# Performance work log

Measured on AMD Instinct MI355X. Metric: run time of the kernel, lower is better.

The kernel has to match this reference:

```python
import jax, jax.numpy as jnp
import numpy as np

N_HEADS = 8
N_LEVELS = 1
N_POINTS = 4
D_MODEL = 256
BATCH = 2
H0, W0 = 100, 150
LS = H0 * W0
LQ = 15000


def layer_norm(x, g, b, eps=1e-5):
    m = jnp.mean(x, -1, keepdims=True)
    v = jnp.var(x, -1, keepdims=True)
    return (x - m) * jax.lax.rsqrt(v + eps) * g + b


def bilinear_sample(v, Hl, Wl, loc):
    # v: [N, Hl*Wl, Hh, D] level features; loc in [0,1]: [N, Lq, Hh, P, 2] (x, y)
    Nb, _, Hh, D = v.shape
    Lq, P = loc.shape[1], loc.shape[3]
    x = loc[..., 0] * Wl - 0.5           # align_corners=False grid_sample convention
    y = loc[..., 1] * Hl - 0.5
    x0 = jnp.floor(x); y0 = jnp.floor(y)
    lx = (x - x0).transpose(0, 2, 1, 3)[..., None]   # [N,Hh,Lq,P,1]
    ly = (y - y0).transpose(0, 2, 1, 3)[..., None]
    x0i = x0.astype(jnp.int32); y0i = y0.astype(jnp.int32)
    vh = v.transpose(0, 2, 1, 3)                      # [N,Hh,Hl*Wl,D]

    def gather(xi, yi):
        valid = (xi >= 0) & (xi < Wl) & (yi >= 0) & (yi < Hl)   # zero padding
        idx = jnp.clip(yi, 0, Hl - 1) * Wl + jnp.clip(xi, 0, Wl - 1)
        idxf = idx.transpose(0, 2, 1, 3).reshape(Nb, Hh, Lq * P)
        g = jnp.take_along_axis(vh, idxf[..., None], axis=2).reshape(Nb, Hh, Lq, P, D)
        return g * valid.transpose(0, 2, 1, 3)[..., None]

    g00 = gather(x0i, y0i)
    g10 = gather(x0i + 1, y0i)
    g01 = gather(x0i, y0i + 1)
    g11 = gather(x0i + 1, y0i + 1)
    return (g00 * (1 - lx) * (1 - ly) + g10 * lx * (1 - ly)
            + g01 * (1 - lx) * ly + g11 * lx * ly)   # [N,Hh,Lq,P,D]


def ms_deform_attn(q, reference_points, src, shapes_np, starts_np, padding_mask,
                   W_val, b_val, W_off, b_off, W_attn, b_attn, W_out, b_out):
    Nb, Lq, C = q.shape
    Hh, D, L, P = N_HEADS, C // N_HEADS, N_LEVELS, N_POINTS
    value = src @ W_val + b_val
    value = jnp.where(padding_mask[..., None], 0.0, value).reshape(Nb, -1, Hh, D)
    offsets = (q @ W_off + b_off).reshape(Nb, Lq, Hh, L, P, 2)
    aw = jax.nn.softmax((q @ W_attn + b_attn).reshape(Nb, Lq, Hh, L * P), -1)
    aw = aw.reshape(Nb, Lq, Hh, L, P)
    # offset normalizer is (W, H) per level
    norm = jnp.asarray(shapes_np[:, ::-1].copy(), dtype=q.dtype)   # [L,2]
    loc = reference_points[:, :, None, :, None, :] + offsets / norm[None, None, None, :, None, :]
    out = 0.0
    for l in range(L):
        Hl, Wl = int(shapes_np[l, 0]), int(shapes_np[l, 1])
        s = int(starts_np[l])
        sampled = bilinear_sample(value[:, s:s + Hl * Wl], Hl, Wl, loc[:, :, :, l])
        out = out + jnp.sum(sampled * aw[:, :, :, l].transpose(0, 2, 1, 3)[..., None], axis=3)
    out = out.transpose(0, 2, 1, 3).reshape(Nb, Lq, C)
    return out @ W_out + b_out


def reference(tgt, query_pos, src_pos, tgt_spatial_shapes, reference_points,
              depth_reference_points, src, src_spatial_shapes, frame_start_index,
              src_padding_mask,
              W_dsa, b_dsa, g_nds, b_nds, W_off, b_off, W_attn, b_attn,
              W_val, b_val, W_out, b_out, W_csa, b_csa, g_n1, b_n1,
              W_ff, b_ff, g_n3, b_n3):
    ss = np.asarray(src_spatial_shapes)      # static level shapes
    starts = np.asarray(frame_start_index)
    # depth scale adaptation
    src_a = layer_norm(src @ W_dsa + b_dsa, g_nds, b_nds)
    q = tgt + query_pos
    tgt2 = ms_deform_attn(q, reference_points, src_a, ss, starts, src_padding_mask,
                          W_val, b_val, W_off, b_off, W_attn, b_attn, W_out, b_out)
    tgt2 = tgt2 @ W_csa + b_csa
    t = layer_norm(tgt + tgt2, g_n1, b_n1)
    # FFN: single linear d_model->d_model with exact GELU (per source code)
    ff = jax.nn.gelu(t @ W_ff + b_ff, approximate=False)
    return layer_norm(t + ff, g_n3, b_n3)


def setup_inputs() -> dict:
    key = jax.random.key(0)
    ks = jax.random.split(key, 24)
    C = D_MODEL
    Hh, L, P = N_HEADS, N_LEVELS, N_POINTS

    def lin(k, fin, fout, scale=None):
        s = (1.0 / np.sqrt(fin)) if scale is None else scale
        return (jax.random.normal(k, (fin, fout), jnp.float32) * s).astype(jnp.float32)

    inp = {}
    inp['tgt'] = jax.random.normal(ks[0], (BATCH, LQ, C), jnp.float32)
    inp['query_pos'] = 0.1 * jax.random.normal(ks[1], (BATCH, LQ, C), jnp.float32)
    inp['src_pos'] = 0.1 * jax.random.normal(ks[2], (BATCH, LS, C), jnp.float32)
    inp['tgt_spatial_shapes'] = jnp.array([[H0, W0]], jnp.int32)
    inp['reference_points'] = jax.random.uniform(ks[3], (BATCH, LQ, L, 2), jnp.float32)
    inp['depth_reference_points'] = jax.random.uniform(ks[4], (BATCH, LQ, 1, 2), jnp.float32)
    inp['src'] = jax.random.normal(ks[5], (BATCH, LS, C), jnp.float32)
    inp['src_spatial_shapes'] = jnp.array([[H0, W0]], jnp.int32)
    inp['frame_start_index'] = jnp.array([0], jnp.int32)
    inp['src_padding_mask'] = jnp.zeros((BATCH, LS), jnp.bool_)
    # parameters
    inp['W_dsa'] = lin(ks[6], C, C); inp['b_dsa'] = jnp.zeros((C,), jnp.float32)
    inp['g_nds'] = jnp.ones((C,), jnp.float32); inp['b_nds'] = jnp.zeros((C,), jnp.float32)
    inp['W_off'] = lin(ks[7], C, Hh * L * P * 2, scale=0.01)
    inp['b_off'] = 0.5 * jax.random.normal(ks[8], (Hh * L * P * 2,), jnp.float32)
    inp['W_attn'] = lin(ks[9], C, Hh * L * P)
    inp['b_attn'] = jnp.zeros((Hh * L * P,), jnp.float32)
    inp['W_val'] = lin(ks[10], C, C); inp['b_val'] = jnp.zeros((C,), jnp.float32)
    inp['W_out'] = lin(ks[11], C, C); inp['b_out'] = jnp.zeros((C,), jnp.float32)
    inp['W_csa'] = lin(ks[12], C, C); inp['b_csa'] = jnp.zeros((C,), jnp.float32)
    inp['g_n1'] = jnp.ones((C,), jnp.float32); inp['b_n1'] = jnp.zeros((C,), jnp.float32)
    inp['W_ff'] = lin(ks[13], C, C); inp['b_ff'] = jnp.zeros((C,), jnp.float32)
    inp['g_n3'] = jnp.ones((C,), jnp.float32); inp['b_n3'] = jnp.zeros((C,), jnp.float32)
    return inp
```

## Files before the change

kernel.cpp:

```cpp
#include <hip/hip_runtime.h>
#include <hip/hip_bf16.h>
#include <math.h>

#define LQ   15000
#define LS_  15000
#define NB   2
#define ROWS (NB*LQ)
#define HGT  100
#define WID  150
#define KDIM 256

typedef __attribute__((ext_vector_type(8))) short bf16x8;
typedef __attribute__((ext_vector_type(4))) float f32x4;

enum { EP_BIAS_F32 = 0, EP_LN_BF = 1, EP_MASK_HM = 2, EP_RES_LN_BF = 3, EP_GELU_RES_LN_F32 = 4 };
enum { AM_BF16 = 0, AM_F32 = 1, AM_F32SUM = 2 };

__device__ inline short f2bf(float x) {
    __hip_bfloat16 h = __float2bfloat16(x);
    return *reinterpret_cast<short*>(&h);
}
__device__ inline unsigned pack2bf(float a, float b) {
    return ((unsigned)(unsigned short)f2bf(a)) | (((unsigned)(unsigned short)f2bf(b)) << 16);
}
__device__ inline float bf2f(short s) {
    return __uint_as_float(((unsigned)(unsigned short)s) << 16);
}
__device__ inline float gelu_exact(float x) {
    return 0.5f * x * (1.f + erff(x * 0.70710678118654752440f));
}

template<int NT, int EPI, int AMODE>
__global__ __launch_bounds__(256) void mfma_gemm(
    const void* __restrict__ Ap, const void* __restrict__ Ap2,
    const short* __restrict__ WT,
    const float* __restrict__ bias, void* __restrict__ Out,
    const void* __restrict__ Res, const unsigned char* __restrict__ mask,
    const float* __restrict__ lng, const float* __restrict__ lnb, int M)
{
    constexpr int BN = NT * 16;
    __shared__ short As[64][40];
    __shared__ short Bs[BN][40];
    __shared__ float sbias[BN], sg[BN], sb2[BN];

    const int tid  = threadIdx.x;
    const int bm0  = blockIdx.x * 64;
    const int wave = tid >> 6, lane = tid & 63;
    const int quad = lane >> 4, c = lane & 15;

    if (tid < BN) {
        sbias[tid] = bias ? bias[tid] : 0.f;
        if (EPI == EP_LN_BF || EPI == EP_RES_LN_BF || EPI == EP_GELU_RES_LN_F32) {
            sg[tid] = lng[tid]; sb2[tid] = lnb[tid];
        }
    }

    f32x4 acc[NT];
    #pragma unroll
    for (int t = 0; t < NT; ++t) acc[t] = (f32x4){0.f, 0.f, 0.f, 0.f};

    for (int k0 = 0; k0 < KDIM; k0 += 32) {
        if (AMODE != AM_BF16) {
            const float* A  = (const float*)Ap;
            const float* A2 = (const float*)Ap2;
            #pragma unroll
            for (int it = 0; it < 2; ++it) {
                int f = it * 256 + tid; int m = f >> 3; int ko = (f & 7) * 4;
                int r = bm0 + m; if (r > M - 1) r = M - 1;
                float4 v = *(const float4*)&A[(size_t)r * KDIM + k0 + ko];
                if (AMODE == AM_F32SUM) {
                    float4 w = *(const float4*)&A2[(size_t)r * KDIM + k0 + ko];
                    v.x += w.x; v.y += w.y; v.z += w.z; v.w += w.w;
                }
                int2 p; p.x = pack2bf(v.x, v.y); p.y = pack2bf(v.z, v.w);
                *(int2*)&As[m][ko] = p;
            }
        } else {
            const short* A = (const short*)Ap;
            int m = tid >> 2; int ko = (tid & 3) * 8;
            int r = bm0 + m; if (r > M - 1) r = M - 1;
            *(int4*)&As[m][ko] = *(const int4*)&A[(size_t)r * KDIM + k0 + ko];
        }
        #pragma unroll
        for (int it = 0; it < (BN * 4 + 255) / 256; ++it) {
            int f = it * 256 + tid;
            if (f < BN * 4) {
                int n = f >> 2; int ko = (f & 3) * 8;
                *(int4*)&Bs[n][ko] = *(const int4*)&WT[(size_t)n * KDIM + k0 + ko];
            }
        }
        __syncthreads();
        bf16x8 a = *(const bf16x8*)&As[wave * 16 + c][quad * 8];
        #pragma unroll
        for (int t = 0; t < NT; ++t) {
            bf16x8 b = *(const bf16x8*)&Bs[t * 16 + c][quad * 8];
            acc[t] = __builtin_amdgcn_mfma_f32_16x16x32_bf16(a, b, acc[t], 0, 0, 0);
        }
        __syncthreads();
    }

    const int r0 = bm0 + wave * 16 + quad * 4;
    if constexpr (EPI == EP_BIAS_F32) {
        float* O = (float*)Out;
        #pragma unroll
        for (int reg = 0; reg < 4; ++reg) {
            int r = r0 + reg;
            if (r < M) {
                #pragma unroll
                for (int t = 0; t < NT; ++t)
                    O[(size_t)r * BN + t * 16 + c] = acc[t][reg] + sbias[t * 16 + c];
            }
        }
    } else if constexpr (EPI == EP_MASK_HM) {
        short* O = (short*)Out;
        #pragma unroll
        for (int reg = 0; reg < 4; ++reg) {
            int r = r0 + reg;
            if (r < M) {
                float mz = mask[r] ? 0.f : 1.f;
                int n = (r >= LS_) ? 1 : 0;
                int s = r - n * LS_;
                #pragma unroll
                for (int t = 0; t < NT; ++t) {
                    int col = t * 16 + c;
                    int h = col >> 5, d = col & 31;
                    O[(((size_t)n * 8 + h) * LS_ + s) * 32 + d] =
                        f2bf((acc[t][reg] + sbias[col]) * mz);
                }
            }
        }
    } else {
        #pragma unroll
        for (int reg = 0; reg < 4; ++reg) {
            int r = r0 + reg;
            int rl = (r < M) ? r : (M - 1);
            float s = 0.f, sq = 0.f;
            #pragma unroll
            for (int t = 0; t < NT; ++t) {
                float v = acc[t][reg] + sbias[t * 16 + c];
                if constexpr (EPI == EP_GELU_RES_LN_F32) {
                    v = gelu_exact(v);
                    v += bf2f(((const short*)Res)[(size_t)rl * 256 + t * 16 + c]);
                } else if constexpr (EPI == EP_RES_LN_BF) {
                    v += ((const float*)Res)[(size_t)rl * 256 + t * 16 + c];
                }
                acc[t][reg] = v;
                s += v; sq += v * v;
            }
            #pragma unroll
            for (int o = 1; o < 16; o <<= 1) {
                s  += __shfl_xor(s,  o, 64);
                sq += __shfl_xor(sq, o, 64);
            }
            float mean = s * (1.f / 256.f);
            float var  = sq * (1.f / 256.f) - mean * mean;
            float rs   = rsqrtf(var + 1e-5f);
            if (r < M) {
                #pragma unroll
                for (int t = 0; t < NT; ++t) {
                    float o = (acc[t][reg] - mean) * rs * sg[t * 16 + c] + sb2[t * 16 + c];
                    if constexpr (EPI == EP_GELU_RES_LN_F32)
                        ((float*)Out)[(size_t)r * 256 + t * 16 + c] = o;
                    else
                        ((short*)Out)[(size_t)r * 256 + t * 16 + c] = f2bf(o);
                }
            }
        }
    }
}

__global__ __launch_bounds__(256) void transp_cvt(const float* __restrict__ W, short* __restrict__ WT)
{
    __shared__ float tile[64][65];
    int bx = blockIdx.x * 64, by = blockIdx.y * 64;
    int tid = threadIdx.x;
    #pragma unroll
    for (int it = 0; it < 4; ++it) {
        int f = it * 256 + tid; int i = f >> 4; int j = (f & 15) * 4;
        float4 v = *(const float4*)&W[(size_t)(by + i) * 256 + bx + j];
        tile[i][j] = v.x; tile[i][j + 1] = v.y; tile[i][j + 2] = v.z; tile[i][j + 3] = v.w;
    }
    __syncthreads();
    #pragma unroll
    for (int it = 0; it < 16; ++it) {
        int f = it * 256 + tid; int nl = f >> 6; int kl = f & 63;
        WT[(size_t)(bx + nl) * 256 + by + kl] = f2bf(tile[kl][nl]);
    }
}

__global__ __launch_bounds__(256) void wc_kernel(
    const float* __restrict__ W_out, const float* __restrict__ W_csa, short* __restrict__ WT_c)
{
    int k = blockIdx.x, n = threadIdx.x;
    float s = 0.f;
    for (int j = 0; j < 256; ++j)
        s = fmaf(W_out[(size_t)k * 256 + j], W_csa[(size_t)j * 256 + n], s);
    WT_c[(size_t)n * 256 + k] = f2bf(s);
}

__global__ __launch_bounds__(256) void bias_combine_kernel(
    const float* __restrict__ b_out, const float* __restrict__ W_csa,
    const float* __restrict__ b_csa, float* __restrict__ bc)
{
    int j = threadIdx.x;
    float s = b_csa[j];
    for (int k = 0; k < 256; ++k) s = fmaf(b_out[k], W_csa[(size_t)k * 256 + j], s);
    bc[j] = s;
}

__global__ __launch_bounds__(256) void pack_oa(
    const float* __restrict__ W_off, const float* __restrict__ W_attn,
    const float* __restrict__ b_off, const float* __restrict__ b_attn,
    short* __restrict__ WT_oa, float* __restrict__ b_oa)
{
    int j = blockIdx.x, k = threadIdx.x;
    float v = (j < 64) ? W_off[(size_t)k * 64 + j] : W_attn[(size_t)k * 32 + (j - 64)];
    WT_oa[(size_t)j * 256 + k] = f2bf(v);
    if (k == 0) b_oa[j] = (j < 64) ? b_off[j] : b_attn[j - 64];
}

__global__ __launch_bounds__(256) void deform_sample(
    const short* __restrict__ value,
    const float* __restrict__ S_oa,
    const float* __restrict__ refp,
    short* __restrict__ out)
{
    int grp = blockIdx.x * 32 + (threadIdx.x >> 3);
    int c4  = threadIdx.x & 7;
    int h = grp & 7;
    int r = grp >> 3;
    int n = (r >= LS_) ? 1 : 0;

    const float* row = S_oa + (size_t)r * 96;
    float rx = refp[(size_t)r * 2 + 0], ry = refp[(size_t)r * 2 + 1];
    float4 oA = *(const float4*)&row[h * 8];
    float4 oB = *(const float4*)&row[h * 8 + 4];
    float4 lg = *(const float4*)&row[64 + h * 4];

    float mx = fmaxf(fmaxf(lg.x, lg.y), fmaxf(lg.z, lg.w));
    float e0 = expf(lg.x - mx), e1 = expf(lg.y - mx), e2 = expf(lg.z - mx), e3 = expf(lg.w - mx);
    float inv = 1.f / (e0 + e1 + e2 + e3);
    float aw[4] = {e0 * inv, e1 * inv, e2 * inv, e3 * inv};
    float ox[4] = {oA.x, oA.z, oB.x, oB.z};
    float oy[4] = {oA.y, oA.w, oB.y, oB.w};

    const short* vb = value + (((size_t)n * 8 + h) * LS_) * 32 + c4 * 4;
    float a0 = 0.f, a1 = 0.f, a2 = 0.f, a3 = 0.f;

    #pragma unroll
    for (int p = 0; p < 4; ++p) {
        float x = rx * (float)WID + ox[p] - 0.5f;
        float y = ry * (float)HGT + oy[p] - 0.5f;
        float x0f = floorf(x), y0f = floorf(y);
        float lx = x - x0f, ly = y - y0f;
        int x0 = (int)x0f, y0 = (int)y0f;
        int x1 = x0 + 1, y1 = y0 + 1;
        bool vx0 = (x0 >= 0) & (x0 < WID), vx1 = (x1 >= 0) & (x1 < WID);
        bool vy0 = (y0 >= 0) & (y0 < HGT), vy1 = (y1 >= 0) & (y1 < HGT);
        float w00 = (vx0 & vy0) ? (1.f - lx) * (1.f - ly) * aw[p] : 0.f;
        float w10 = (vx1 & vy0) ? lx * (1.f - ly) * aw[p] : 0.f;
        float w01 = (vx0 & vy1) ? (1.f - lx) * ly * aw[p] : 0.f;
        float w11 = (vx1 & vy1) ? lx * ly * aw[p] : 0.f;
        int xc0 = min(max(x0, 0), WID - 1), xc1 = min(max(x1, 0), WID - 1);
        int yc0 = min(max(y0, 0), HGT - 1), yc1 = min(max(y1, 0), HGT - 1);
        int2 v00 = *(const int2*)&vb[(size_t)(yc0 * WID + xc0) * 32];
        int2 v10 = *(const int2*)&vb[(size_t)(yc0 * WID + xc1) * 32];
        int2 v01 = *(const int2*)&vb[(size_t)(yc1 * WID + xc0) * 32];
        int2 v11 = *(const int2*)&vb[(size_t)(yc1 * WID + xc1) * 32];
        a0 += w00 * __uint_as_float(((unsigned)v00.x) << 16)
            + w10 * __uint_as_float(((unsigned)v10.x) << 16)
            + w01 * __uint_as_float(((unsigned)v01.x) << 16)
            + w11 * __uint_as_float(((unsigned)v11.x) << 16);
        a1 += w00 * __uint_as_float(v00.x & 0xffff0000u)
            + w10 * __uint_as_float(v10.x & 0xffff0000u)
            + w01 * __uint_as_float(v01.x & 0xffff0000u)
            + w11 * __uint_as_float(v11.x & 0xffff0000u);
        a2 += w00 * __uint_as_float(((unsigned)v00.y) << 16)
            + w10 * __uint_as_float(((unsigned)v10.y) << 16)
            + w01 * __uint_as_float(((unsigned)v01.y) << 16)
            + w11 * __uint_as_float(((unsigned)v11.y) << 16);
        a3 += w00 * __uint_as_float(v00.y & 0xffff0000u)
            + w10 * __uint_as_float(v10.y & 0xffff0000u)
            + w01 * __uint_as_float(v01.y & 0xffff0000u)
            + w11 * __uint_as_float(v11.y & 0xffff0000u);
    }
    int2 o;
    o.x = pack2bf(a0, a1);
    o.y = pack2bf(a2, a3);
    *(int2*)&out[(size_t)r * 256 + h * 32 + c4 * 4] = o;
}

extern "C" void kernel_launch(void* const* d_in, const int* in_sizes, int n_in,
                              void* d_out, int out_size, void* d_ws, size_t ws_size,
                              hipStream_t stream)
{
    const float* tgt       = (const float*)d_in[0];
    const float* query_pos = (const float*)d_in[1];
    const float* refp      = (const float*)d_in[4];
    const float* src       = (const float*)d_in[6];
    const unsigned char* mask = (const unsigned char*)d_in[9];
    const float* W_dsa  = (const float*)d_in[10]; const float* b_dsa  = (const float*)d_in[11];
    const float* g_nds  = (const float*)d_in[12]; const float* b_nds  = (const float*)d_in[13];
    const float* W_off  = (const float*)d_in[14]; const float* b_off  = (const float*)d_in[15];
    const float* W_attn = (const float*)d_in[16]; const float* b_attn = (const float*)d_in[17];
    const float* W_val  = (const float*)d_in[18]; const float* b_val  = (const float*)d_in[19];
    const float* W_out  = (const float*)d_in[20]; const float* b_out  = (const float*)d_in[21];
    const float* W_csa  = (const float*)d_in[22]; const float* b_csa  = (const float*)d_in[23];
    const float* g_n1   = (const float*)d_in[24]; const float* b_n1   = (const float*)d_in[25];
    const float* W_ff   = (const float*)d_in[26]; const float* b_ff   = (const float*)d_in[27];
    const float* g_n3   = (const float*)d_in[28]; const float* b_n3   = (const float*)d_in[29];
    float* out = (float*)d_out;

    short* bf0   = (short*)d_ws;
    short* bf1   = bf0 + (size_t)ROWS * 256;
    short* bf2   = bf1 + (size_t)ROWS * 256;
    float* S_oa  = (float*)(bf2 + (size_t)ROWS * 256);
    short* WT_dsa = (short*)(S_oa + (size_t)ROWS * 96);
    short* WT_val = WT_dsa + 65536;
    short* WT_c   = WT_val + 65536;
    short* WT_ff  = WT_c + 65536;
    short* WT_oa  = WT_ff + 65536;
    float* bc     = (float*)(WT_oa + 96 * 256);
    float* b_oa   = bc + 256;

    dim3 blk(256);
    const int GB = (ROWS + 63) / 64;

    transp_cvt<<<dim3(4, 4), blk, 0, stream>>>(W_dsa, WT_dsa);
    transp_cvt<<<dim3(4, 4), blk, 0, stream>>>(W_val, WT_val);
    transp_cvt<<<dim3(4, 4), blk, 0, stream>>>(W_ff,  WT_ff);
    wc_kernel<<<256, blk, 0, stream>>>(W_out, W_csa, WT_c);
    bias_combine_kernel<<<1, blk, 0, stream>>>(b_out, W_csa, b_csa, bc);
    pack_oa<<<96, blk, 0, stream>>>(W_off, W_attn, b_off, b_attn, WT_oa, b_oa);

    mfma_gemm<16, EP_LN_BF, AM_F32><<<GB, blk, 0, stream>>>(
        src, nullptr, WT_dsa, b_dsa, bf0, nullptr, nullptr, g_nds, b_nds, ROWS);
    mfma_gemm<16, EP_MASK_HM, AM_BF16><<<GB, blk, 0, stream>>>(
        bf0, nullptr, WT_val, b_val, bf2, nullptr, mask, nullptr, nullptr, ROWS);
    mfma_gemm<6, EP_BIAS_F32, AM_F32SUM><<<GB, blk, 0, stream>>>(
        tgt, query_pos, WT_oa, b_oa, S_oa, nullptr, nullptr, nullptr, nullptr, ROWS);
    deform_sample<<<ROWS * 8 / 32, blk, 0, stream>>>(bf2, S_oa, refp, bf0);
    mfma_gemm<16, EP_RES_LN_BF, AM_BF16><<<GB, blk, 0, stream>>>(
        bf0, nullptr, WT_c, bc, bf1, tgt, nullptr, g_n1, b_n1, ROWS);
    mfma_gemm<16, EP_GELU_RES_LN_F32, AM_BF16><<<GB, blk, 0, stream>>>(
        bf1, nullptr, WT_ff, b_ff, out, bf1, nullptr, g_n3, b_n3, ROWS);
}
```

Measured before the change: 347.0 us.

## Fuse GEMM pairs and offset GEMM with deformable sampling; merge prep kernels

Chains of two GEMMs are fused into one kernel: the first GEMM plus layernorm result stays in LDS as bf16 and feeds the second GEMM, so the intermediate activation never goes through global memory. The offset/attention GEMM is fused with bilinear sampling through an LDS staging tile. The weight preparation kernels are merged into one launch. This cuts several full-size intermediate round trips and launches. The cost is much larger LDS per block (about 60KB), which lowers occupancy, and more serialized work per block.

```diff
diff --git a/kernel.cpp b/kernel.cpp
--- a/kernel.cpp
+++ b/kernel.cpp
@@ -8,13 +8,9 @@
 #define ROWS (NB*LQ)
 #define HGT  100
 #define WID  150
-#define KDIM 256
 
 typedef __attribute__((ext_vector_type(8))) short bf16x8;
 typedef __attribute__((ext_vector_type(4))) float f32x4;
-
-enum { EP_BIAS_F32 = 0, EP_LN_BF = 1, EP_MASK_HM = 2, EP_RES_LN_BF = 3, EP_GELU_RES_LN_F32 = 4 };
-enum { AM_BF16 = 0, AM_F32 = 1, AM_F32SUM = 2 };
 
 __device__ inline short f2bf(float x) {
     __hip_bfloat16 h = __float2bfloat16(x);
@@ -30,48 +26,45 @@
     return 0.5f * x * (1.f + erff(x * 0.70710678118654752440f));
 }
 
-template<int NT, int EPI, int AMODE>
-__global__ __launch_bounds__(256) void mfma_gemm(
-    const void* __restrict__ Ap, const void* __restrict__ Ap2,
-    const short* __restrict__ WT,
-    const float* __restrict__ bias, void* __restrict__ Out,
-    const void* __restrict__ Res, const unsigned char* __restrict__ mask,
-    const float* __restrict__ lng, const float* __restrict__ lnb, int M)
+template<int MODE>
+__global__ __launch_bounds__(256) void fused2(
+    const void* __restrict__ Ap,
+    const short* __restrict__ W1T, const float* __restrict__ bias1,
+    const float* __restrict__ res1,
+    const float* __restrict__ g1v, const float* __restrict__ b1v,
+    const short* __restrict__ W2T, const float* __restrict__ bias2,
+    void* __restrict__ Out,
+    const unsigned char* __restrict__ mask,
+    const float* __restrict__ g2v, const float* __restrict__ b2v,
+    int M)
 {
-    constexpr int BN = NT * 16;
     __shared__ short As[64][40];
-    __shared__ short Bs[BN][40];
-    __shared__ float sbias[BN], sg[BN], sb2[BN];
-
-    const int tid  = threadIdx.x;
-    const int bm0  = blockIdx.x * 64;
+    __shared__ short Bs[256][40];
+    __shared__ short T[64][264];
+    __shared__ float s_b1[256], s_g1[256], s_bb1[256], s_b2[256], s_g2[256], s_bb2[256];
+
+    const int tid = threadIdx.x;
+    const int bm0 = blockIdx.x * 64;
     const int wave = tid >> 6, lane = tid & 63;
     const int quad = lane >> 4, c = lane & 15;
 
-    if (tid < BN) {
-        sbias[tid] = bias ? bias[tid] : 0.f;
-        if (EPI == EP_LN_BF || EPI == EP_RES_LN_BF || EPI == EP_GELU_RES_LN_F32) {
-            sg[tid] = lng[tid]; sb2[tid] = lnb[tid];
-        }
-    }
-
-    f32x4 acc[NT];
+    s_b1[tid] = bias1[tid];
+    s_g1[tid] = g1v[tid]; s_bb1[tid] = b1v[tid];
+    s_b2[tid] = bias2[tid];
+    if (MODE == 1) { s_g2[tid] = g2v[tid]; s_bb2[tid] = b2v[tid]; }
+
+    f32x4 acc[16];
     #pragma unroll
-    for (int t = 0; t < NT; ++t) acc[t] = (f32x4){0.f, 0.f, 0.f, 0.f};
-
-    for (int k0 = 0; k0 < KDIM; k0 += 32) {
-        if (AMODE != AM_BF16) {
-            const float* A  = (const float*)Ap;
-            const float* A2 = (const float*)Ap2;
+    for (int t = 0; t < 16; ++t) acc[t] = (f32x4){0.f, 0.f, 0.f, 0.f};
+
+    for (int k0 = 0; k0 < 256; k0 += 32) {
+        if (MODE == 0) {
+            const float* A = (const float*)Ap;
             #pragma unroll
             for (int it = 0; it < 2; ++it) {
                 int f = it * 256 + tid; int m = f >> 3; int ko = (f & 7) * 4;
                 int r = bm0 + m; if (r > M - 1) r = M - 1;
-                float4 v = *(const float4*)&A[(size_t)r * KDIM + k0 + ko];
-                if (AMODE == AM_F32SUM) {
-                    float4 w = *(const float4*)&A2[(size_t)r * KDIM + k0 + ko];
-                    v.x += w.x; v.y += w.y; v.z += w.z; v.w += w.w;
-                }
+                float4 v = *(const float4*)&A[(size_t)r * 256 + k0 + ko];
                 int2 p; p.x = pack2bf(v.x, v.y); p.y = pack2bf(v.z, v.w);
                 *(int2*)&As[m][ko] = p;
             }
@@ -79,215 +72,297 @@
             const short* A = (const short*)Ap;
             int m = tid >> 2; int ko = (tid & 3) * 8;
             int r = bm0 + m; if (r > M - 1) r = M - 1;
-            *(int4*)&As[m][ko] = *(const int4*)&A[(size_t)r * KDIM + k0 + ko];
-        }
-        #pragma unroll
-        for (int it = 0; it < (BN * 4 + 255) / 256; ++it) {
-            int f = it * 256 + tid;
-            if (f < BN * 4) {
-                int n = f >> 2; int ko = (f & 3) * 8;
-                *(int4*)&Bs[n][ko] = *(const int4*)&WT[(size_t)n * KDIM + k0 + ko];
-            }
+            *(int4*)&As[m][ko] = *(const int4*)&A[(size_t)r * 256 + k0 + ko];
+        }
+        #pragma unroll
+        for (int it = 0; it < 4; ++it) {
+            int f = it * 256 + tid; int n = f >> 2; int ko = (f & 3) * 8;
+            *(int4*)&Bs[n][ko] = *(const int4*)&W1T[(size_t)n * 256 + k0 + ko];
         }
         __syncthreads();
         bf16x8 a = *(const bf16x8*)&As[wave * 16 + c][quad * 8];
         #pragma unroll
-        for (int t = 0; t < NT; ++t) {
+        for (int t = 0; t < 16; ++t) {
             bf16x8 b = *(const bf16x8*)&Bs[t * 16 + c][quad * 8];
             acc[t] = __builtin_amdgcn_mfma_f32_16x16x32_bf16(a, b, acc[t], 0, 0, 0);
         }
         __syncthreads();
     }
 
-    const int r0 = bm0 + wave * 16 + quad * 4;
-    if constexpr (EPI == EP_BIAS_F32) {
-        float* O = (float*)Out;
+    {
+        const int rb = wave * 16 + quad * 4;
         #pragma unroll
         for (int reg = 0; reg < 4; ++reg) {
-            int r = r0 + reg;
-            if (r < M) {
-                #pragma unroll
-                for (int t = 0; t < NT; ++t)
-                    O[(size_t)r * BN + t * 16 + c] = acc[t][reg] + sbias[t * 16 + c];
-            }
-        }
-    } else if constexpr (EPI == EP_MASK_HM) {
+            int rloc = rb + reg;
+            int rg = bm0 + rloc; int rgl = (rg < M) ? rg : (M - 1);
+            float s = 0.f, sq = 0.f;
+            float vv[16];
+            #pragma unroll
+            for (int t = 0; t < 16; ++t) {
+                float v = acc[t][reg] + s_b1[t * 16 + c];
+                if (MODE == 1) v += res1[(size_t)rgl * 256 + t * 16 + c];
+                vv[t] = v; s += v; sq += v * v;
+            }
+            #pragma unroll
+            for (int o = 1; o < 16; o <<= 1) {
+                s += __shfl_xor(s, o, 64); sq += __shfl_xor(sq, o, 64);
+            }
+            float mean = s * (1.f / 256.f);
+            float var  = sq * (1.f / 256.f) - mean * mean;
+            float rs   = rsqrtf(var + 1e-5f);
+            #pragma unroll
+            for (int t = 0; t < 16; ++t)
+                T[rloc][t * 16 + c] = f2bf((vv[t] - mean) * rs * s_g1[t * 16 + c] + s_bb1[t * 16 + c]);
+        }
+    }
+    __syncthreads();
+
+    #pragma unroll
+    for (int t = 0; t < 16; ++t) acc[t] = (f32x4){0.f, 0.f, 0.f, 0.f};
+    for (int k0 = 0; k0 < 256; k0 += 32) {
+        #pragma unroll
+        for (int it = 0; it < 4; ++it) {
+            int f = it * 256 + tid; int n = f >> 2; int ko = (f & 3) * 8;
+            *(int4*)&Bs[n][ko] = *(const int4*)&W2T[(size_t)n * 256 + k0 + ko];
+        }
+        __syncthreads();
+        bf16x8 a = *(const bf16x8*)&T[wave * 16 + c][k0 + quad * 8];
+        #pragma unroll
+        for (int t = 0; t < 16; ++t) {
+            bf16x8 b = *(const bf16x8*)&Bs[t * 16 + c][quad * 8];
+            acc[t] = __builtin_amdgcn_mfma_f32_16x16x32_bf16(a, b, acc[t], 0, 0, 0);
+        }
+        __syncthreads();
+    }
+
+    const int rb = wave * 16 + quad * 4;
+    if constexpr (MODE == 0) {
         short* O = (short*)Out;
         #pragma unroll
         for (int reg = 0; reg < 4; ++reg) {
-            int r = r0 + reg;
+            int rloc = rb + reg; int r = bm0 + rloc;
             if (r < M) {
                 float mz = mask[r] ? 0.f : 1.f;
                 int n = (r >= LS_) ? 1 : 0;
-                int s = r - n * LS_;
+                int sidx = r - n * LS_;
                 #pragma unroll
-                for (int t = 0; t < NT; ++t) {
-                    int col = t * 16 + c;
-                    int h = col >> 5, d = col & 31;
-                    O[(((size_t)n * 8 + h) * LS_ + s) * 32 + d] =
-                        f2bf((acc[t][reg] + sbias[col]) * mz);
+                for (int t = 0; t < 16; ++t) {
+                    int col = t * 16 + c; int h = col >> 5, d = col & 31;
+                    O[(((size_t)n * 8 + h) * LS_ + sidx) * 32 + d] =
+                        f2bf((acc[t][reg] + s_b2[col]) * mz);
                 }
             }
         }
     } else {
+        float* O = (float*)Out;
         #pragma unroll
         for (int reg = 0; reg < 4; ++reg) {
-            int r = r0 + reg;
-            int rl = (r < M) ? r : (M - 1);
+            int rloc = rb + reg; int r = bm0 + rloc;
             float s = 0.f, sq = 0.f;
-            #pragma unroll
-            for (int t = 0; t < NT; ++t) {
-                float v = acc[t][reg] + sbias[t * 16 + c];
-                if constexpr (EPI == EP_GELU_RES_LN_F32) {
-                    v = gelu_exact(v);
-                    v += bf2f(((const short*)Res)[(size_t)rl * 256 + t * 16 + c]);
-                } else if constexpr (EPI == EP_RES_LN_BF) {
-                    v += ((const float*)Res)[(size_t)rl * 256 + t * 16 + c];
-                }
-                acc[t][reg] = v;
-                s += v; sq += v * v;
+            float vv[16];
+            #pragma unroll
+            for (int t = 0; t < 16; ++t) {
+                int col = t * 16 + c;
+                float v = gelu_exact(acc[t][reg] + s_b2[col]) + bf2f(T[rloc][col]);
+                vv[t] = v; s += v; sq += v * v;
             }
             #pragma unroll
             for (int o = 1; o < 16; o <<= 1) {
-                s  += __shfl_xor(s,  o, 64);
-                sq += __shfl_xor(sq, o, 64);
+                s += __shfl_xor(s, o, 64); sq += __shfl_xor(sq, o, 64);
             }
             float mean = s * (1.f / 256.f);
             float var  = sq * (1.f / 256.f) - mean * mean;
             float rs   = rsqrtf(var + 1e-5f);
             if (r < M) {
                 #pragma unroll
-                for (int t = 0; t < NT; ++t) {
-                    float o = (acc[t][reg] - mean) * rs * sg[t * 16 + c] + sb2[t * 16 + c];
-                    if constexpr (EPI == EP_GELU_RES_LN_F32)
-                        ((float*)Out)[(size_t)r * 256 + t * 16 + c] = o;
-                    else
-                        ((short*)Out)[(size_t)r * 256 + t * 16 + c] = f2bf(o);
+                for (int t = 0; t < 16; ++t) {
+                    int col = t * 16 + c;
+                    O[(size_t)r * 256 + col] = (vv[t] - mean) * rs * s_g2[col] + s_bb2[col];
                 }
             }
         }
     }
 }
 
-__global__ __launch_bounds__(256) void transp_cvt(const float* __restrict__ W, short* __restrict__ WT)
+__global__ __launch_bounds__(256) void fused_oa_sample(
+    const float* __restrict__ tgt, const float* __restrict__ qpos,
+    const short* __restrict__ WToa, const float* __restrict__ b_oa,
+    const short* __restrict__ value,
+    const float* __restrict__ refp,
+    short* __restrict__ out, int M)
+{
+    __shared__ short As[64][40];
+    __shared__ short Bs[96][40];
+    __shared__ float Ss[64][100];
+    __shared__ float sb[96];
+
+    const int tid = threadIdx.x;
+    const int bm0 = blockIdx.x * 64;
+    const int wave = tid >> 6, lane = tid & 63;
+    const int quad = lane >> 4, c = lane & 15;
+
+    if (tid < 96) sb[tid] = b_oa[tid];
+
+    f32x4 acc[6];
+    #pragma unroll
+    for (int t = 0; t < 6; ++t) acc[t] = (f32x4){0.f, 0.f, 0.f, 0.f};
+
+    for (int k0 = 0; k0 < 256; k0 += 32) {
+        #pragma unroll
+        for (int it = 0; it < 2; ++it) {
+            int f = it * 256 + tid; int m = f >> 3; int ko = (f & 7) * 4;
+            int r = bm0 + m; if (r > M - 1) r = M - 1;
+            float4 v = *(const float4*)&tgt[(size_t)r * 256 + k0 + ko];
+            float4 w = *(const float4*)&qpos[(size_t)r * 256 + k0 + ko];
+            v.x += w.x; v.y += w.y; v.z += w.z; v.w += w.w;
+            int2 p; p.x = pack2bf(v.x, v.y); p.y = pack2bf(v.z, v.w);
+            *(int2*)&As[m][ko] = p;
+        }
+        #pragma unroll
+        for (int it = 0; it < 2; ++it) {
+            int f = it * 256 + tid;
+            if (f < 384) {
+                int n = f >> 2; int ko = (f & 3) * 8;
+                *(int4*)&Bs[n][ko] = *(const int4*)&WToa[(size_t)n * 256 + k0 + ko];
+            }
+        }
+        __syncthreads();
+        bf16x8 a = *(const bf16x8*)&As[wave * 16 + c][quad * 8];
+        #pragma unroll
+        for (int t = 0; t < 6; ++t) {
+            bf16x8 b = *(const bf16x8*)&Bs[t * 16 + c][quad * 8];
+            acc[t] = __builtin_amdgcn_mfma_f32_16x16x32_bf16(a, b, acc[t], 0, 0, 0);
+        }
+        __syncthreads();
+    }
+    {
+        const int rbq = wave * 16 + quad * 4;
+        #pragma unroll
+        for (int reg = 0; reg < 4; ++reg) {
+            int rloc = rbq + reg;
+            #pragma unroll
+            for (int t = 0; t < 6; ++t)
+                Ss[rloc][t * 16 + c] = acc[t][reg] + sb[t * 16 + c];
+        }
+    }
+    __syncthreads();
+
+    const int c4 = tid & 7;
+    #pragma unroll 2
+    for (int it = 0; it < 16; ++it) {
+        int g = it * 32 + (tid >> 3);
+        int rloc = g >> 3, h = g & 7;
+        int r = bm0 + rloc;
+        bool ok = r < M;
+        int rr = ok ? r : (M - 1);
+        int n = (rr >= LS_) ? 1 : 0;
+        float rx = refp[(size_t)rr * 2 + 0], ry = refp[(size_t)rr * 2 + 1];
+        float4 oA = *(const float4*)&Ss[rloc][h * 8];
+        float4 oB = *(const float4*)&Ss[rloc][h * 8 + 4];
+        float4 lg = *(const float4*)&Ss[rloc][64 + h * 4];
+
+        float mx = fmaxf(fmaxf(lg.x, lg.y), fmaxf(lg.z, lg.w));
+        float e0 = expf(lg.x - mx), e1 = expf(lg.y - mx), e2 = expf(lg.z - mx), e3 = expf(lg.w - mx);
+        float inv = 1.f / (e0 + e1 + e2 + e3);
+        float aw[4] = {e0 * inv, e1 * inv, e2 * inv, e3 * inv};
+        float ox[4] = {oA.x, oA.z, oB.x, oB.z};
+        float oy[4] = {oA.y, oA.w, oB.y, oB.w};
+
+        const short* vb = value + (((size_t)n * 8 + h) * LS_) * 32 + c4 * 4;
+        float a0 = 0.f, a1 = 0.f, a2 = 0.f, a3 = 0.f;
+        #pragma unroll
+        for (int p = 0; p < 4; ++p) {
+            float x = rx * (float)WID + ox[p] - 0.5f;
+            float y = ry * (float)HGT + oy[p] - 0.5f;
+            float x0f = floorf(x), y0f = floorf(y);
+            float lx = x - x0f, ly = y - y0f;
+            int x0 = (int)x0f, y0 = (int)y0f;
+            int x1 = x0 + 1, y1 = y0 + 1;
+            bool vx0 = (x0 >= 0) & (x0 < WID), vx1 = (x1 >= 0) & (x1 < WID);
+            bool vy0 = (y0 >= 0) & (y0 < HGT), vy1 = (y1 >= 0) & (y1 < HGT);
+            float w00 = (vx0 & vy0) ? (1.f - lx) * (1.f - ly) * aw[p] : 0.f;
+            float w10 = (vx1 & vy0) ? lx * (1.f - ly) * aw[p] : 0.f;
+            float w01 = (vx0 & vy1) ? (1.f - lx) * ly * aw[p] : 0.f;
+            float w11 = (vx1 & vy1) ? lx * ly * aw[p] : 0.f;
+            int xc0 = min(max(x0, 0), WID - 1), xc1 = min(max(x1, 0), WID - 1);
+            int yc0 = min(max(y0, 0), HGT - 1), yc1 = min(max(y1, 0), HGT - 1);
+            int2 v00 = *(const int2*)&vb[(size_t)(yc0 * WID + xc0) * 32];
+            int2 v10 = *(const int2*)&vb[(size_t)(yc0 * WID + xc1) * 32];
+            int2 v01 = *(const int2*)&vb[(size_t)(yc1 * WID + xc0) * 32];
+            int2 v11 = *(const int2*)&vb[(size_t)(yc1 * WID + xc1) * 32];
+            a0 += w00 * __uint_as_float(((unsigned)v00.x) << 16)
+                + w10 * __uint_as_float(((unsigned)v10.x) << 16)
+                + w01 * __uint_as_float(((unsigned)v01.x) << 16)
+                + w11 * __uint_as_float(((unsigned)v11.x) << 16);
+            a1 += w00 * __uint_as_float(v00.x & 0xffff0000u)
+                + w10 * __uint_as_float(v10.x & 0xffff0000u)
+                + w01 * __uint_as_float(v01.x & 0xffff0000u)
+                + w11 * __uint_as_float(v11.x & 0xffff0000u);
+            a2 += w00 * __uint_as_float(((unsigned)v00.y) << 16)
+                + w10 * __uint_as_float(((unsigned)v10.y) << 16)
+                + w01 * __uint_as_float(((unsigned)v01.y) << 16)
+                + w11 * __uint_as_float(((unsigned)v11.y) << 16);
+            a3 += w00 * __uint_as_float(v00.y & 0xffff0000u)
+                + w10 * __uint_as_float(v10.y & 0xffff0000u)
+                + w01 * __uint_as_float(v01.y & 0xffff0000u)
+                + w11 * __uint_as_float(v11.y & 0xffff0000u);
+        }
+        if (ok) {
+            int2 o;
+            o.x = pack2bf(a0, a1);
+            o.y = pack2bf(a2, a3);
+            *(int2*)&out[(size_t)r * 256 + h * 32 + c4 * 4] = o;
+        }
+    }
+}
+
+__global__ __launch_bounds__(256) void prep_all(
+    const float* __restrict__ W_dsa, const float* __restrict__ W_val,
+    const float* __restrict__ W_ff,  const float* __restrict__ W_out,
+    const float* __restrict__ W_csa, const float* __restrict__ b_out,
+    const float* __restrict__ b_csa, const float* __restrict__ W_off,
+    const float* __restrict__ W_attn, const float* __restrict__ b_off,
+    const float* __restrict__ b_attn,
+    short* __restrict__ WT_dsa, short* __restrict__ WT_val, short* __restrict__ WT_ff,
+    short* __restrict__ WT_c, float* __restrict__ bc,
+    short* __restrict__ WT_oa, float* __restrict__ b_oa)
 {
     __shared__ float tile[64][65];
-    int bx = blockIdx.x * 64, by = blockIdx.y * 64;
-    int tid = threadIdx.x;
-    #pragma unroll
-    for (int it = 0; it < 4; ++it) {
-        int f = it * 256 + tid; int i = f >> 4; int j = (f & 15) * 4;
-        float4 v = *(const float4*)&W[(size_t)(by + i) * 256 + bx + j];
-        tile[i][j] = v.x; tile[i][j + 1] = v.y; tile[i][j + 2] = v.z; tile[i][j + 3] = v.w;
-    }
-    __syncthreads();
-    #pragma unroll
-    for (int it = 0; it < 16; ++it) {
-        int f = it * 256 + tid; int nl = f >> 6; int kl = f & 63;
-        WT[(size_t)(bx + nl) * 256 + by + kl] = f2bf(tile[kl][nl]);
-    }
-}
-
-__global__ __launch_bounds__(256) void wc_kernel(
-    const float* __restrict__ W_out, const float* __restrict__ W_csa, short* __restrict__ WT_c)
-{
-    int k = blockIdx.x, n = threadIdx.x;
-    float s = 0.f;
-    for (int j = 0; j < 256; ++j)
-        s = fmaf(W_out[(size_t)k * 256 + j], W_csa[(size_t)j * 256 + n], s);
-    WT_c[(size_t)n * 256 + k] = f2bf(s);
-}
-
-__global__ __launch_bounds__(256) void bias_combine_kernel(
-    const float* __restrict__ b_out, const float* __restrict__ W_csa,
-    const float* __restrict__ b_csa, float* __restrict__ bc)
-{
-    int j = threadIdx.x;
-    float s = b_csa[j];
-    for (int k = 0; k < 256; ++k) s = fmaf(b_out[k], W_csa[(size_t)k * 256 + j], s);
-    bc[j] = s;
-}
-
-__global__ __launch_bounds__(256) void pack_oa(
-    const float* __restrict__ W_off, const float* __restrict__ W_attn,
-    const float* __restrict__ b_off, const float* __restrict__ b_attn,
-    short* __restrict__ WT_oa, float* __restrict__ b_oa)
-{
-    int j = blockIdx.x, k = threadIdx.x;
-    float v = (j < 64) ? W_off[(size_t)k * 64 + j] : W_attn[(size_t)k * 32 + (j - 64)];
-    WT_oa[(size_t)j * 256 + k] = f2bf(v);
-    if (k == 0) b_oa[j] = (j < 64) ? b_off[j] : b_attn[j - 64];
-}
-
-__global__ __launch_bounds__(256) void deform_sample(
-    const short* __restrict__ value,
-    const float* __restrict__ S_oa,
-    const float* __restrict__ refp,
-    short* __restrict__ out)
-{
-    int grp = blockIdx.x * 32 + (threadIdx.x >> 3);
-    int c4  = threadIdx.x & 7;
-    int h = grp & 7;
-    int r = grp >> 3;
-    int n = (r >= LS_) ? 1 : 0;
-
-    const float* row = S_oa + (size_t)r * 96;
-    float rx = refp[(size_t)r * 2 + 0], ry = refp[(size_t)r * 2 + 1];
-    float4 oA = *(const float4*)&row[h * 8];
-    float4 oB = *(const float4*)&row[h * 8 + 4];
-    float4 lg = *(const float4*)&row[64 + h * 4];
-
-    float mx = fmaxf(fmaxf(lg.x, lg.y), fmaxf(lg.z, lg.w));
-    float e0 = expf(lg.x - mx), e1 = expf(lg.y - mx), e2 = expf(lg.z - mx), e3 = expf(lg.w - mx);
-    float inv = 1.f / (e0 + e1 + e2 + e3);
-    float aw[4] = {e0 * inv, e1 * inv, e2 * inv, e3 * inv};
-    float ox[4] = {oA.x, oA.z, oB.x, oB.z};
-    float oy[4] = {oA.y, oA.w, oB.y, oB.w};
-
-    const short* vb = value + (((size_t)n * 8 + h) * LS_) * 32 + c4 * 4;
-    float a0 = 0.f, a1 = 0.f, a2 = 0.f, a3 = 0.f;
-
-    #pragma unroll
-    for (int p = 0; p < 4; ++p) {
-        float x = rx * (float)WID + ox[p] - 0.5f;
-        float y = ry * (float)HGT + oy[p] - 0.5f;
-        float x0f = floorf(x), y0f = floorf(y);
-        float lx = x - x0f, ly = y - y0f;
-        int x0 = (int)x0f, y0 = (int)y0f;
-        int x1 = x0 + 1, y1 = y0 + 1;
-        bool vx0 = (x0 >= 0) & (x0 < WID), vx1 = (x1 >= 0) & (x1 < WID);
-        bool vy0 = (y0 >= 0) & (y0 < HGT), vy1 = (y1 >= 0) & (y1 < HGT);
-        float w00 = (vx0 & vy0) ? (1.f - lx) * (1.f - ly) * aw[p] : 0.f;
-        float w10 = (vx1 & vy0) ? lx * (1.f - ly) * aw[p] : 0.f;
-        float w01 = (vx0 & vy1) ? (1.f - lx) * ly * aw[p] : 0.f;
-        float w11 = (vx1 & vy1) ? lx * ly * aw[p] : 0.f;
-        int xc0 = min(max(x0, 0), WID - 1), xc1 = min(max(x1, 0), WID - 1);
-        int yc0 = min(max(y0, 0), HGT - 1), yc1 = min(max(y1, 0), HGT - 1);
-        int2 v00 = *(const int2*)&vb[(size_t)(yc0 * WID + xc0) * 32];
-        int2 v10 = *(const int2*)&vb[(size_t)(yc0 * WID + xc1) * 32];
-        int2 v01 = *(const int2*)&vb[(size_t)(yc1 * WID + xc0) * 32];
-        int2 v11 = *(const int2*)&vb[(size_t)(yc1 * WID + xc1) * 32];
-        a0 += w00 * __uint_as_float(((unsigned)v00.x) << 16)
-            + w10 * __uint_as_float(((unsigned)v10.x) << 16)
-            + w01 * __uint_as_float(((unsigned)v01.x) << 16)
-            + w11 * __uint_as_float(((unsigned)v11.x) << 16);
-        a1 += w00 * __uint_as_float(v00.x & 0xffff0000u)
-            + w10 * __uint_as_float(v10.x & 0xffff0000u)
-            + w01 * __uint_as_float(v01.x & 0xffff0000u)
-            + w11 * __uint_as_float(v11.x & 0xffff0000u);
-        a2 += w00 * __uint_as_float(((unsigned)v00.y) << 16)
-            + w10 * __uint_as_float(((unsigned)v10.y) << 16)
-            + w01 * __uint_as_float(((unsigned)v01.y) << 16)
-            + w11 * __uint_as_float(((unsigned)v11.y) << 16);
-        a3 += w00 * __uint_as_float(v00.y & 0xffff0000u)
-            + w10 * __uint_as_float(v10.y & 0xffff0000u)
-            + w01 * __uint_as_float(v01.y & 0xffff0000u)
-            + w11 * __uint_as_float(v11.y & 0xffff0000u);
-    }
-    int2 o;
-    o.x = pack2bf(a0, a1);
-    o.y = pack2bf(a2, a3);
-    *(int2*)&out[(size_t)r * 256 + h * 32 + c4 * 4] = o;
+    const int b = blockIdx.x, tid = threadIdx.x;
+    if (b < 48) {
+        const float* W = (b < 16) ? W_dsa : (b < 32) ? W_val : W_ff;
+        short* WT = (b < 16) ? WT_dsa : (b < 32) ? WT_val : WT_ff;
+        int t = b & 15; int bx = (t & 3) * 64, by = (t >> 2) * 64;
+        #pragma unroll
+        for (int it = 0; it < 4; ++it) {
+            int f = it * 256 + tid; int i = f >> 4; int j = (f & 15) * 4;
+            float4 v = *(const float4*)&W[(size_t)(by + i) * 256 + bx + j];
+            tile[i][j] = v.x; tile[i][j + 1] = v.y; tile[i][j + 2] = v.z; tile[i][j + 3] = v.w;
+        }
+        __syncthreads();
+        #pragma unroll
+        for (int it = 0; it < 16; ++it) {
+            int f = it * 256 + tid; int nl = f >> 6; int kl = f & 63;
+            WT[(size_t)(bx + nl) * 256 + by + kl] = f2bf(tile[kl][nl]);
+        }
+    } else if (b < 304) {
+        int k = b - 48, n = tid;
+        float s = 0.f;
+        for (int j = 0; j < 256; ++j)
+            s = fmaf(W_out[(size_t)k * 256 + j], W_csa[(size_t)j * 256 + n], s);
+        WT_c[(size_t)n * 256 + k] = f2bf(s);
+    } else if (b == 304) {
+        int j = tid;
+        float s = b_csa[j];
+        for (int k = 0; k < 256; ++k)
+            s = fmaf(b_out[k], W_csa[(size_t)k * 256 + j], s);
+        bc[j] = s;
+    } else {
+        int j = b - 305, k = tid;
+        float v = (j < 64) ? W_off[(size_t)k * 64 + j] : W_attn[(size_t)k * 32 + (j - 64)];
+        WT_oa[(size_t)j * 256 + k] = f2bf(v);
+        if (k == 0) b_oa[j] = (j < 64) ? b_off[j] : b_attn[j - 64];
+    }
 }
 
 extern "C" void kernel_launch(void* const* d_in, const int* in_sizes, int n_in,
@@ -311,37 +386,31 @@
     const float* g_n3   = (const float*)d_in[28]; const float* b_n3   = (const float*)d_in[29];
     float* out = (float*)d_out;
 
-    short* bf0   = (short*)d_ws;
-    short* bf1   = bf0 + (size_t)ROWS * 256;
-    short* bf2   = bf1 + (size_t)ROWS * 256;
-    float* S_oa  = (float*)(bf2 + (size_t)ROWS * 256);
-    short* WT_dsa = (short*)(S_oa + (size_t)ROWS * 96);
-    short* WT_val = WT_dsa + 65536;
-    short* WT_c   = WT_val + 65536;
-    short* WT_ff  = WT_c + 65536;
-    short* WT_oa  = WT_ff + 65536;
-    float* bc     = (float*)(WT_oa + 96 * 256);
-    float* b_oa   = bc + 256;
+    short* attn_out = (short*)d_ws;
+    short* value    = attn_out + (size_t)ROWS * 256;
+    short* WT_dsa   = value + (size_t)ROWS * 256;
+    short* WT_val   = WT_dsa + 65536;
+    short* WT_ff    = WT_val + 65536;
+    short* WT_c     = WT_ff + 65536;
+    short* WT_oa    = WT_c + 65536;
+    float* bc       = (float*)(WT_oa + 96 * 256);
+    float* b_oa     = bc + 256;
 
     dim3 blk(256);
     const int GB = (ROWS + 63) / 64;
 
-    transp_cvt<<<dim3(4, 4), blk, 0, stream>>>(W_dsa, WT_dsa);
-    transp_cvt<<<dim3(4, 4), blk, 0, stream>>>(W_val, WT_val);
-    transp_cvt<<<dim3(4, 4), blk, 0, stream>>>(W_ff,  WT_ff);
-    wc_kernel<<<256, blk, 0, stream>>>(W_out, W_csa, WT_c);
-    bias_combine_kernel<<<1, blk, 0, stream>>>(b_out, W_csa, b_csa, bc);
-    pack_oa<<<96, blk, 0, stream>>>(W_off, W_attn, b_off, b_attn, WT_oa, b_oa);
-
-    mfma_gemm<16, EP_LN_BF, AM_F32><<<GB, blk, 0, stream>>>(
-        src, nullptr, WT_dsa, b_dsa, bf0, nullptr, nullptr, g_nds, b_nds, ROWS);
-    mfma_gemm<16, EP_MASK_HM, AM_BF16><<<GB, blk, 0, stream>>>(
-        bf0, nullptr, WT_val, b_val, bf2, nullptr, mask, nullptr, nullptr, ROWS);
-    mfma_gemm<6, EP_BIAS_F32, AM_F32SUM><<<GB, blk, 0, stream>>>(
-        tgt, query_pos, WT_oa, b_oa, S_oa, nullptr, nullptr, nullptr, nullptr, ROWS);
-    deform_sample<<<ROWS * 8 / 32, blk, 0, stream>>>(bf2, S_oa, refp, bf0);
-    mfma_gemm<16, EP_RES_LN_BF, AM_BF16><<<GB, blk, 0, stream>>>(
-        bf0, nullptr, WT_c, bc, bf1, tgt, nullptr, g_n1, b_n1, ROWS);
-    mfma_gemm<16, EP_GELU_RES_LN_F32, AM_BF16><<<GB, blk, 0, stream>>>(
-        bf1, nullptr, WT_ff, b_ff, out, bf1, nullptr, g_n3, b_n3, ROWS);
-}
+    prep_all<<<401, blk, 0, stream>>>(
+        W_dsa, W_val, W_ff, W_out, W_csa, b_out, b_csa, W_off, W_attn, b_off, b_attn,
+        WT_dsa, WT_val, WT_ff, WT_c, bc, WT_oa, b_oa);
+
+    fused2<0><<<GB, blk, 0, stream>>>(
+        src, WT_dsa, b_dsa, nullptr, g_nds, b_nds,
+        WT_val, b_val, value, mask, nullptr, nullptr, ROWS);
+
+    fused_oa_sample<<<GB, blk, 0, stream>>>(
+        tgt, query_pos, WT_oa, b_oa, value, refp, attn_out, ROWS);
+
+    fused2<1><<<GB, blk, 0, stream>>>(
+        attn_out, WT_c, bc, tgt, g_n1, b_n1,
+        WT_ff, b_ff, out, nullptr, g_n3, b_n3, ROWS);
+}
```

After: 332.7 us. 4.1% less time.
